# Performance work log

Hardware: AMD Instinct MI355X
Metric: run time of the kernel (lower is better)

## Reference

```python
import jax, jax.numpy as jnp
import numpy as np

H = 1024      # hidden_size
L = 2         # num_layers
V = 32000     # src/tgt vocab
S = 512       # source length
T = 512       # target length
BOS = 0


def _gru_cell(h, x, Wih, Whh, bih, bhh):
    # h,x: [H]; Wih,Whh: [3H,H]; gate order r,z,n (PyTorch convention)
    gi = Wih @ x + bih
    gh = Whh @ h + bhh
    i_r, i_z, i_n = jnp.split(gi, 3)
    h_r, h_z, h_n = jnp.split(gh, 3)
    r = jax.nn.sigmoid(i_r + h_r)
    z = jax.nn.sigmoid(i_z + h_z)
    n = jnp.tanh(i_n + r * h_n)
    return (1.0 - z) * n + z * h


def _run_gru(xs, h0, Wih, Whh, bih, bhh):
    # xs: [T,H] embedded tokens; h0: [L,H]; weights: [L,3H,H]/[L,3H]
    n_layers = Wih.shape[0]

    def step(h, x):
        inp = x
        new_h = []
        for l in range(n_layers):  # small fixed layer loop
            hl = _gru_cell(h[l], inp, Wih[l], Whh[l], bih[l], bhh[l])
            new_h.append(hl)
            inp = hl
        return jnp.stack(new_h), inp  # carry [L,H], emit top-layer hidden

    return jax.lax.scan(step, h0, xs)


def setup_inputs() -> dict:
    key = jax.random.key(0)
    ks = jax.random.split(key, 16)
    sc = 1.0 / np.sqrt(H)

    def gw(k, shape):
        return (jax.random.normal(k, shape, dtype=jnp.float32) * sc)

    return {
        "src_tokens": jax.random.randint(ks[0], (S,), 0, V),
        "tgt_tokens": jax.random.randint(ks[1], (T,), 0, V),
        "src_emb": gw(ks[2], (V, H)),
        "tgt_emb": gw(ks[3], (V, H)),
        "enc_Wih": gw(ks[4], (L, 3 * H, H)),
        "enc_Whh": gw(ks[5], (L, 3 * H, H)),
        "enc_bih": gw(ks[6], (L, 3 * H)),
        "enc_bhh": gw(ks[7], (L, 3 * H)),
        "dec_Wih": gw(ks[8], (L, 3 * H, H)),
        "dec_Whh": gw(ks[9], (L, 3 * H, H)),
        "dec_bih": gw(ks[10], (L, 3 * H)),
        "dec_bhh": gw(ks[11], (L, 3 * H)),
        "out_W": gw(ks[12], (V, H)),
        "out_b": jnp.zeros((V,), dtype=jnp.float32),
    }


def reference(src_tokens, tgt_tokens, src_emb, tgt_emb,
              enc_Wih, enc_Whh, enc_bih, enc_bhh,
              dec_Wih, dec_Whh, dec_bih, dec_bhh,
              out_W, out_b):
    # ---- encoder: embed + L-layer GRU over source ----
    enc_x = src_emb[src_tokens]                       # [S,H]
    h0 = jnp.zeros((enc_Wih.shape[0], src_emb.shape[1]), src_emb.dtype)
    h_enc, _ = _run_gru(enc_x, h0, enc_Wih, enc_Whh, enc_bih, enc_bhh)
    # ---- decoder: teacher-forced inputs [BOS, tgt[:-1]] ----
    dec_in = jnp.concatenate(
        [jnp.array([BOS], dtype=tgt_tokens.dtype), tgt_tokens[:-1]])
    dec_x = tgt_emb[dec_in]                           # [T,H]
    _, dec_top = _run_gru(dec_x, h_enc, dec_Wih, dec_Whh, dec_bih, dec_bhh)
    logits = dec_top @ out_W.T + out_b                # [T,V]
    logp = jax.nn.log_softmax(logits, axis=-1)
    return logp[:, None, None, :]                     # [T,1,1,V] like torch.stack
```

## Files before the change

kernel.cpp:

```cpp
#include <hip/hip_runtime.h>
#include <hip/hip_bf16.h>
#include <math.h>


#define HID 1024
#define NSTEP 512
#define VOCAB 32000
#define SPIN_LIMIT 50000
typedef unsigned long long u64;

__device__ __forceinline__ u64 pack_hv(float v, unsigned tag) {
    return ((u64)tag << 32) | (u64)__float_as_uint(v);
}

__device__ __forceinline__ void poll16(const u64* __restrict__ row, unsigned want,
                                       float* v, int lane) {
    u64 p[16];
    int iter = 0;
    for (;;) {
        bool ok = true;
#pragma unroll
        for (int q = 0; q < 16; ++q) {
            p[q] = __hip_atomic_load((u64*)(row + q * 64 + lane),
                                     __ATOMIC_RELAXED, __HIP_MEMORY_SCOPE_AGENT);
            ok = ok && ((unsigned)(p[q] >> 32) == want);
        }
        if (ok) break;
        if (++iter >= SPIN_LIMIT) {
#pragma unroll
            for (int q = 0; q < 16; ++q) v[q] = __uint_as_float(0x7fc00000u);
            return;
        }
        __builtin_amdgcn_s_sleep(1);
    }
#pragma unroll
    for (int q = 0; q < 16; ++q)
        v[q] = __uint_as_float((unsigned)(p[q] & 0xffffffffu));
}

__global__ __launch_bounds__(256) void gather_embed(
    const int* __restrict__ src_tok, const int* __restrict__ tgt_tok,
    const float* __restrict__ src_emb, const float* __restrict__ tgt_emb,
    float* __restrict__ enc_x, float* __restrict__ dec_x) {
    int b = blockIdx.x, tid = threadIdx.x;
    int tok;
    const float* src;
    float* dst;
    if (b < 512) {
        tok = src_tok[b];
        src = src_emb;
        dst = enc_x + (size_t)b * HID;
    } else {
        int t = b - 512;
        tok = (t == 0) ? 0 : tgt_tok[t - 1];
        src = tgt_emb;
        dst = dec_x + (size_t)t * HID;
    }
    float4 v = *(const float4*)(src + (size_t)tok * HID + tid * 4);
    *(float4*)(dst + tid * 4) = v;
}

__global__ __launch_bounds__(256, 1) void gru_persist(
    const float* __restrict__ enc_x, const float* __restrict__ dec_x,
    const float* __restrict__ eWih, const float* __restrict__ eWhh,
    const float* __restrict__ eBih, const float* __restrict__ eBhh,
    const float* __restrict__ dWih, const float* __restrict__ dWhh,
    const float* __restrict__ dBih, const float* __restrict__ dBhh,
    u64* H0, u64* H1, u64* D0, u64* D1, float* __restrict__ D1f) {
    const int tid = threadIdx.x;
    const int wave = tid >> 6, lane = tid & 63;
    const int role = blockIdx.x >> 7;
    const int wl = blockIdx.x & 127;
    const int j0 = wl * 8;

    __shared__ float dots[48];
    __shared__ float sbias[48];

    float wreg[12][16];
    float hprev = 0.f;

#pragma unroll 1
    for (int phase = 0; phase < 2; ++phase) {
        const bool dec = (phase == 1);
        const float* Wih = (dec ? dWih : eWih) + (size_t)role * 3 * HID * HID;
        const float* Whh = (dec ? dWhh : eWhh) + (size_t)role * 3 * HID * HID;
        const float* bih = (dec ? dBih : eBih) + (size_t)role * 3 * HID;
        const float* bhh = (dec ? dBhh : eBhh) + (size_t)role * 3 * HID;
        u64* hch = dec ? (role ? D1 : D0) : (role ? H1 : H0);
        const unsigned tagOut = dec ? (role ? 4u : 3u) : (role ? 2u : 1u);
        const float* xf = dec ? dec_x : enc_x;
        const u64* xt = dec ? D0 : H0;
        const unsigned tagX = dec ? 3u : 1u;
        const u64* hinit = role ? (H1 + (size_t)(NSTEP - 1) * HID)
                                : (H0 + (size_t)(NSTEP - 1) * HID);
        const unsigned tagInit = role ? 2u : 1u;

        __syncthreads();
#pragma unroll
        for (int r = 0; r < 12; ++r) {
            int R = wave * 12 + r;
            int m = (R < 24) ? R : R - 24;
            const float* base = ((R < 24) ? Wih : Whh) +
                                (size_t)((m >> 3) * HID + j0 + (m & 7)) * HID;
#pragma unroll
            for (int q = 0; q < 16; ++q) wreg[r][q] = base[q * 64 + lane];
        }
        if (tid < 48) {
            int m = (tid < 24) ? tid : tid - 24;
            sbias[tid] = ((tid < 24) ? bih : bhh)[(m >> 3) * HID + j0 + (m & 7)];
        }
        __syncthreads();

#pragma unroll 1
        for (int t = 0; t < NSTEP; ++t) {
            float v[16];
            if (wave < 2) {
                if (role == 0) {
                    const float* xr = xf + (size_t)t * HID;
#pragma unroll
                    for (int q = 0; q < 16; ++q) v[q] = xr[q * 64 + lane];
                } else {
                    poll16(xt + (size_t)t * HID, tagX, v, lane);
                }
            } else {
                if (t > 0) {
                    poll16(hch + (size_t)(t - 1) * HID, tagOut, v, lane);
                } else if (dec) {
                    poll16(hinit, tagInit, v, lane);
                } else {
#pragma unroll
                    for (int q = 0; q < 16; ++q) v[q] = 0.f;
                }
            }

            float part[12];
#pragma unroll
            for (int r = 0; r < 12; ++r) {
                float a = 0.f;
#pragma unroll
                for (int q = 0; q < 16; ++q) a = fmaf(wreg[r][q], v[q], a);
                part[r] = a;
            }
#pragma unroll
            for (int off = 1; off < 64; off <<= 1) {
#pragma unroll
                for (int r = 0; r < 12; ++r) part[r] += __shfl_xor(part[r], off);
            }
            if (lane == 0) {
#pragma unroll
                for (int r = 0; r < 12; ++r) dots[wave * 12 + r] = part[r];
            }
            __syncthreads();

            if (tid < 8) {
                const int jj = tid;
                float ir = dots[jj] + sbias[jj];
                float iz = dots[8 + jj] + sbias[8 + jj];
                float in_ = dots[16 + jj] + sbias[16 + jj];
                float hr = dots[24 + jj] + sbias[24 + jj];
                float hz = dots[32 + jj] + sbias[32 + jj];
                float hn = dots[40 + jj] + sbias[40 + jj];
                float rg = 1.f / (1.f + __expf(-(ir + hr)));
                float zg = 1.f / (1.f + __expf(-(iz + hz)));
                float na = in_ + rg * hn;
                float ng = 2.f / (1.f + __expf(-2.f * na)) - 1.f;
                float hnew = (1.f - zg) * ng + zg * hprev;
                hprev = hnew;
                __hip_atomic_store((u64*)(hch + (size_t)t * HID + j0 + jj),
                                   pack_hv(hnew, tagOut),
                                   __ATOMIC_RELAXED, __HIP_MEMORY_SCOPE_AGENT);
                if (dec && role == 1) D1f[(size_t)t * HID + j0 + jj] = hnew;
            }
            __syncthreads();
        }
    }
}

__global__ __launch_bounds__(256) void gemm_out(
    const float* __restrict__ A, const float* __restrict__ B,
    const float* __restrict__ bias, float* __restrict__ C) {
    const int tid = threadIdx.x;
    const int bi = blockIdx.x;
    const int bv = blockIdx.y;
    const int i0 = bi * 64, v0 = bv * 128;
    __shared__ __align__(16) float As[32 * 68];
    __shared__ __align__(16) float Bs[32 * 132];
    const int tr = tid >> 4, tc = tid & 15;
    float c[4][8] = {};

    for (int kk = 0; kk < HID; kk += 32) {
#pragma unroll
        for (int q = 0; q < 2; q++) {
            int id = tid * 2 + q;
            int r = id >> 3, kq = id & 7;
            float4 a = *(const float4*)&A[(size_t)(i0 + r) * HID + kk + kq * 4];
            As[(kq * 4 + 0) * 68 + r] = a.x;
            As[(kq * 4 + 1) * 68 + r] = a.y;
            As[(kq * 4 + 2) * 68 + r] = a.z;
            As[(kq * 4 + 3) * 68 + r] = a.w;
        }
#pragma unroll
        for (int q = 0; q < 4; q++) {
            int id = tid * 4 + q;
            int vr = id >> 3, kq = id & 7;
            float4 b = *(const float4*)&B[(size_t)(v0 + vr) * HID + kk + kq * 4];
            Bs[(kq * 4 + 0) * 132 + vr] = b.x;
            Bs[(kq * 4 + 1) * 132 + vr] = b.y;
            Bs[(kq * 4 + 2) * 132 + vr] = b.z;
            Bs[(kq * 4 + 3) * 132 + vr] = b.w;
        }
        __syncthreads();
#pragma unroll
        for (int k = 0; k < 32; k++) {
            float4 a4 = *(const float4*)&As[k * 68 + tr * 4];
            float4 b0 = *(const float4*)&Bs[k * 132 + tc * 8];
            float4 b1 = *(const float4*)&Bs[k * 132 + tc * 8 + 4];
            float av[4] = {a4.x, a4.y, a4.z, a4.w};
            float bvv[8] = {b0.x, b0.y, b0.z, b0.w, b1.x, b1.y, b1.z, b1.w};
#pragma unroll
            for (int u = 0; u < 4; u++)
#pragma unroll
                for (int w = 0; w < 8; w++) c[u][w] += av[u] * bvv[w];
        }
        __syncthreads();
    }
    float4 bb0 = *(const float4*)&bias[v0 + tc * 8];
    float4 bb1 = *(const float4*)&bias[v0 + tc * 8 + 4];
#pragma unroll
    for (int u = 0; u < 4; u++) {
        int i = i0 + tr * 4 + u;
        float4 o0 = {c[u][0] + bb0.x, c[u][1] + bb0.y, c[u][2] + bb0.z, c[u][3] + bb0.w};
        float4 o1 = {c[u][4] + bb1.x, c[u][5] + bb1.y, c[u][6] + bb1.z, c[u][7] + bb1.w};
        *(float4*)&C[(size_t)i * VOCAB + v0 + tc * 8] = o0;
        *(float4*)&C[(size_t)i * VOCAB + v0 + tc * 8 + 4] = o1;
    }
}

__global__ __launch_bounds__(256) void log_softmax_inplace(float* __restrict__ C) {
    const int row = blockIdx.x;
    const int tid = threadIdx.x;
    float* p = C + (size_t)row * VOCAB;
    float m = -3.4e38f, s = 0.f;
    for (int idx = tid; idx < VOCAB / 4; idx += 256) {
        float4 x = ((const float4*)p)[idx];
        float xv[4] = {x.x, x.y, x.z, x.w};
#pragma unroll
        for (int u = 0; u < 4; u++) {
            float nm = fmaxf(m, xv[u]);
            s = s * __expf(m - nm) + __expf(xv[u] - nm);
            m = nm;
        }
    }
#pragma unroll
    for (int off = 1; off < 64; off <<= 1) {
        float om = __shfl_xor(m, off);
        float os = __shfl_xor(s, off);
        float nm = fmaxf(m, om);
        s = s * __expf(m - nm) + os * __expf(om - nm);
        m = nm;
    }
    __shared__ float sm[4], ss[4], sL;
    int wv = tid >> 6;
    if ((tid & 63) == 0) { sm[wv] = m; ss[wv] = s; }
    __syncthreads();
    if (tid == 0) {
        float M = sm[0], S = ss[0];
        for (int w = 1; w < 4; w++) {
            float nm = fmaxf(M, sm[w]);
            S = S * __expf(M - nm) + ss[w] * __expf(sm[w] - nm);
            M = nm;
        }
        sL = M + logf(S);
    }
    __syncthreads();
    float L = sL;
    for (int idx = tid; idx < VOCAB / 4; idx += 256) {
        float4 x = ((const float4*)p)[idx];
        x.x -= L; x.y -= L; x.z -= L; x.w -= L;
        ((float4*)p)[idx] = x;
    }
}

extern "C" void kernel_launch(void* const* d_in, const int* in_sizes, int n_in,
                              void* d_out, int out_size, void* d_ws, size_t ws_size,
                              hipStream_t stream) {
    const int* src_tok = (const int*)d_in[0];
    const int* tgt_tok = (const int*)d_in[1];
    const float* src_emb = (const float*)d_in[2];
    const float* tgt_emb = (const float*)d_in[3];
    const float* eWih = (const float*)d_in[4];
    const float* eWhh = (const float*)d_in[5];
    const float* eBih = (const float*)d_in[6];
    const float* eBhh = (const float*)d_in[7];
    const float* dWih = (const float*)d_in[8];
    const float* dWhh = (const float*)d_in[9];
    const float* dBih = (const float*)d_in[10];
    const float* dBhh = (const float*)d_in[11];
    const float* out_W = (const float*)d_in[12];
    const float* out_b = (const float*)d_in[13];
    float* out = (float*)d_out;

    char* ws = (char*)d_ws;
    float* enc_x = (float*)(ws);
    float* dec_x = (float*)(ws + (2ull << 20));
    u64* H0 = (u64*)(ws + (4ull << 20));
    u64* H1 = (u64*)(ws + (8ull << 20));
    u64* D0 = (u64*)(ws + (12ull << 20));
    u64* D1 = (u64*)(ws + (16ull << 20));
    float* D1f = (float*)(ws + (20ull << 20));

    hipMemsetAsync(ws + (4ull << 20), 0, 16ull << 20, stream);

    gather_embed<<<1024, 256, 0, stream>>>(src_tok, tgt_tok, src_emb, tgt_emb, enc_x, dec_x);
    gru_persist<<<256, 256, 0, stream>>>(enc_x, dec_x, eWih, eWhh, eBih, eBhh,
                                         dWih, dWhh, dBih, dBhh, H0, H1, D0, D1, D1f);
    gemm_out<<<dim3(8, 250), 256, 0, stream>>>(D1f, out_W, out_b, out);
    log_softmax_inplace<<<512, 256, 0, stream>>>(out);
}
```

Measured before the change: 3.733 ms.

## Precompute layer-0 input projections with batched GEMM, halve layer-0 recurrent work

Layer 0's input projection Wih·x for every timestep is now computed up front with the existing GEMM kernel for both encoder and decoder. The layer-0 recurrent blocks then load only Whh and do 6 dot rows per wave instead of 12, which shortens the serial critical path. Block-to-role mapping is interleaved across XCDs, and the s_sleep in the poll loop is removed so spinning is tighter. The cost is two extra GEMM launches plus more workspace traffic, and busier polling that adds memory pressure.

```diff
diff --git a/kernel.cpp b/kernel.cpp
--- a/kernel.cpp
+++ b/kernel.cpp
@@ -31,7 +31,6 @@
             for (int q = 0; q < 16; ++q) v[q] = __uint_as_float(0x7fc00000u);
             return;
         }
-        __builtin_amdgcn_s_sleep(1);
     }
 #pragma unroll
     for (int q = 0; q < 16; ++q)
@@ -61,7 +60,7 @@
 }
 
 __global__ __launch_bounds__(256, 1) void gru_persist(
-    const float* __restrict__ enc_x, const float* __restrict__ dec_x,
+    const float* __restrict__ gi_e, const float* __restrict__ gi_d,
     const float* __restrict__ eWih, const float* __restrict__ eWhh,
     const float* __restrict__ eBih, const float* __restrict__ eBhh,
     const float* __restrict__ dWih, const float* __restrict__ dWhh,
@@ -69,8 +68,9 @@
     u64* H0, u64* H1, u64* D0, u64* D1, float* __restrict__ D1f) {
     const int tid = threadIdx.x;
     const int wave = tid >> 6, lane = tid & 63;
-    const int role = blockIdx.x >> 7;
-    const int wl = blockIdx.x & 127;
+    const int xcd = blockIdx.x & 7;
+    const int role = (xcd >= 4) ? 1 : 0;
+    const int wl = (blockIdx.x >> 3) * 4 + (xcd & 3);
     const int j0 = wl * 8;
 
     __shared__ float dots[48];
@@ -88,7 +88,7 @@
         const float* bhh = (dec ? dBhh : eBhh) + (size_t)role * 3 * HID;
         u64* hch = dec ? (role ? D1 : D0) : (role ? H1 : H0);
         const unsigned tagOut = dec ? (role ? 4u : 3u) : (role ? 2u : 1u);
-        const float* xf = dec ? dec_x : enc_x;
+        const float* gi = dec ? gi_d : gi_e;
         const u64* xt = dec ? D0 : H0;
         const unsigned tagX = dec ? 3u : 1u;
         const u64* hinit = role ? (H1 + (size_t)(NSTEP - 1) * HID)
@@ -96,33 +96,44 @@
         const unsigned tagInit = role ? 2u : 1u;
 
         __syncthreads();
-#pragma unroll
-        for (int r = 0; r < 12; ++r) {
-            int R = wave * 12 + r;
-            int m = (R < 24) ? R : R - 24;
-            const float* base = ((R < 24) ? Wih : Whh) +
-                                (size_t)((m >> 3) * HID + j0 + (m & 7)) * HID;
-#pragma unroll
-            for (int q = 0; q < 16; ++q) wreg[r][q] = base[q * 64 + lane];
-        }
-        if (tid < 48) {
-            int m = (tid < 24) ? tid : tid - 24;
-            sbias[tid] = ((tid < 24) ? bih : bhh)[(m >> 3) * HID + j0 + (m & 7)];
+        if (role == 0) {
+#pragma unroll
+            for (int r = 0; r < 6; ++r) {
+                int m = wave * 6 + r;
+                const float* base = Whh + (size_t)((m >> 3) * HID + j0 + (m & 7)) * HID;
+#pragma unroll
+                for (int q = 0; q < 16; ++q) wreg[r][q] = base[q * 64 + lane];
+            }
+            if (tid < 24)
+                sbias[tid] = bhh[(tid >> 3) * HID + j0 + (tid & 7)];
+        } else {
+#pragma unroll
+            for (int r = 0; r < 12; ++r) {
+                int R = wave * 12 + r;
+                int m = (R < 24) ? R : R - 24;
+                const float* base = ((R < 24) ? Wih : Whh) +
+                                    (size_t)((m >> 3) * HID + j0 + (m & 7)) * HID;
+#pragma unroll
+                for (int q = 0; q < 16; ++q) wreg[r][q] = base[q * 64 + lane];
+            }
+            if (tid < 48) {
+                int m = (tid < 24) ? tid : tid - 24;
+                sbias[tid] = ((tid < 24) ? bih : bhh)[(m >> 3) * HID + j0 + (m & 7)];
+            }
         }
         __syncthreads();
 
 #pragma unroll 1
         for (int t = 0; t < NSTEP; ++t) {
-            float v[16];
-            if (wave < 2) {
-                if (role == 0) {
-                    const float* xr = xf + (size_t)t * HID;
-#pragma unroll
-                    for (int q = 0; q < 16; ++q) v[q] = xr[q * 64 + lane];
-                } else {
-                    poll16(xt + (size_t)t * HID, tagX, v, lane);
-                }
-            } else {
+            if (role == 0) {
+                float gir = 0.f, giz = 0.f, gin = 0.f;
+                if (tid < 8) {
+                    const float* gp = gi + (size_t)t * 3 * HID + j0 + tid;
+                    gir = gp[0];
+                    giz = gp[HID];
+                    gin = gp[2 * HID];
+                }
+                float v[16];
                 if (t > 0) {
                     poll16(hch + (size_t)(t - 1) * HID, tagOut, v, lane);
                 } else if (dec) {
@@ -131,54 +142,102 @@
 #pragma unroll
                     for (int q = 0; q < 16; ++q) v[q] = 0.f;
                 }
+                float part[6];
+#pragma unroll
+                for (int r = 0; r < 6; ++r) {
+                    float a = 0.f;
+#pragma unroll
+                    for (int q = 0; q < 16; ++q) a = fmaf(wreg[r][q], v[q], a);
+                    part[r] = a;
+                }
+#pragma unroll
+                for (int off = 1; off < 64; off <<= 1) {
+#pragma unroll
+                    for (int r = 0; r < 6; ++r) part[r] += __shfl_xor(part[r], off);
+                }
+                if (lane == 0) {
+#pragma unroll
+                    for (int r = 0; r < 6; ++r) dots[wave * 6 + r] = part[r];
+                }
+                __syncthreads();
+
+                if (tid < 8) {
+                    const int jj = tid;
+                    float hr = dots[jj] + sbias[jj];
+                    float hz = dots[8 + jj] + sbias[8 + jj];
+                    float hn = dots[16 + jj] + sbias[16 + jj];
+                    float rg = 1.f / (1.f + __expf(-(gir + hr)));
+                    float zg = 1.f / (1.f + __expf(-(giz + hz)));
+                    float na = gin + rg * hn;
+                    float ng = 2.f / (1.f + __expf(-2.f * na)) - 1.f;
+                    float hnew = (1.f - zg) * ng + zg * hprev;
+                    hprev = hnew;
+                    __hip_atomic_store((u64*)(hch + (size_t)t * HID + j0 + jj),
+                                       pack_hv(hnew, tagOut),
+                                       __ATOMIC_RELAXED, __HIP_MEMORY_SCOPE_AGENT);
+                }
+                __syncthreads();
+            } else {
+                float v[16];
+                if (wave < 2) {
+                    poll16(xt + (size_t)t * HID, tagX, v, lane);
+                } else {
+                    if (t > 0) {
+                        poll16(hch + (size_t)(t - 1) * HID, tagOut, v, lane);
+                    } else if (dec) {
+                        poll16(hinit, tagInit, v, lane);
+                    } else {
+#pragma unroll
+                        for (int q = 0; q < 16; ++q) v[q] = 0.f;
+                    }
+                }
+                float part[12];
+#pragma unroll
+                for (int r = 0; r < 12; ++r) {
+                    float a = 0.f;
+#pragma unroll
+                    for (int q = 0; q < 16; ++q) a = fmaf(wreg[r][q], v[q], a);
+                    part[r] = a;
+                }
+#pragma unroll
+                for (int off = 1; off < 64; off <<= 1) {
+#pragma unroll
+                    for (int r = 0; r < 12; ++r) part[r] += __shfl_xor(part[r], off);
+                }
+                if (lane == 0) {
+#pragma unroll
+                    for (int r = 0; r < 12; ++r) dots[wave * 12 + r] = part[r];
+                }
+                __syncthreads();
+
+                if (tid < 8) {
+                    const int jj = tid;
+                    float ir = dots[jj] + sbias[jj];
+                    float iz = dots[8 + jj] + sbias[8 + jj];
+                    float in_ = dots[16 + jj] + sbias[16 + jj];
+                    float hr = dots[24 + jj] + sbias[24 + jj];
+                    float hz = dots[32 + jj] + sbias[32 + jj];
+                    float hn = dots[40 + jj] + sbias[40 + jj];
+                    float rg = 1.f / (1.f + __expf(-(ir + hr)));
+                    float zg = 1.f / (1.f + __expf(-(iz + hz)));
+                    float na = in_ + rg * hn;
+                    float ng = 2.f / (1.f + __expf(-2.f * na)) - 1.f;
+                    float hnew = (1.f - zg) * ng + zg * hprev;
+                    hprev = hnew;
+                    __hip_atomic_store((u64*)(hch + (size_t)t * HID + j0 + jj),
+                                       pack_hv(hnew, tagOut),
+                                       __ATOMIC_RELAXED, __HIP_MEMORY_SCOPE_AGENT);
+                    if (dec) D1f[(size_t)t * HID + j0 + jj] = hnew;
+                }
+                __syncthreads();
             }
-
-            float part[12];
-#pragma unroll
-            for (int r = 0; r < 12; ++r) {
-                float a = 0.f;
-#pragma unroll
-                for (int q = 0; q < 16; ++q) a = fmaf(wreg[r][q], v[q], a);
-                part[r] = a;
-            }
-#pragma unroll
-            for (int off = 1; off < 64; off <<= 1) {
-#pragma unroll
-                for (int r = 0; r < 12; ++r) part[r] += __shfl_xor(part[r], off);
-            }
-            if (lane == 0) {
-#pragma unroll
-                for (int r = 0; r < 12; ++r) dots[wave * 12 + r] = part[r];
-            }
-            __syncthreads();
-
-            if (tid < 8) {
-                const int jj = tid;
-                float ir = dots[jj] + sbias[jj];
-                float iz = dots[8 + jj] + sbias[8 + jj];
-                float in_ = dots[16 + jj] + sbias[16 + jj];
-                float hr = dots[24 + jj] + sbias[24 + jj];
-                float hz = dots[32 + jj] + sbias[32 + jj];
-                float hn = dots[40 + jj] + sbias[40 + jj];
-                float rg = 1.f / (1.f + __expf(-(ir + hr)));
-                float zg = 1.f / (1.f + __expf(-(iz + hz)));
-                float na = in_ + rg * hn;
-                float ng = 2.f / (1.f + __expf(-2.f * na)) - 1.f;
-                float hnew = (1.f - zg) * ng + zg * hprev;
-                hprev = hnew;
-                __hip_atomic_store((u64*)(hch + (size_t)t * HID + j0 + jj),
-                                   pack_hv(hnew, tagOut),
-                                   __ATOMIC_RELAXED, __HIP_MEMORY_SCOPE_AGENT);
-                if (dec && role == 1) D1f[(size_t)t * HID + j0 + jj] = hnew;
-            }
-            __syncthreads();
         }
     }
 }
 
 __global__ __launch_bounds__(256) void gemm_out(
     const float* __restrict__ A, const float* __restrict__ B,
-    const float* __restrict__ bias, float* __restrict__ C) {
+    const float* __restrict__ bias, float* __restrict__ C, int ldc) {
     const int tid = threadIdx.x;
     const int bi = blockIdx.x;
     const int bv = blockIdx.y;
@@ -231,8 +290,8 @@
         int i = i0 + tr * 4 + u;
         float4 o0 = {c[u][0] + bb0.x, c[u][1] + bb0.y, c[u][2] + bb0.z, c[u][3] + bb0.w};
         float4 o1 = {c[u][4] + bb1.x, c[u][5] + bb1.y, c[u][6] + bb1.z, c[u][7] + bb1.w};
-        *(float4*)&C[(size_t)i * VOCAB + v0 + tc * 8] = o0;
-        *(float4*)&C[(size_t)i * VOCAB + v0 + tc * 8 + 4] = o1;
+        *(float4*)&C[(size_t)i * ldc + v0 + tc * 8] = o0;
+        *(float4*)&C[(size_t)i * ldc + v0 + tc * 8 + 4] = o1;
     }
 }
 
@@ -308,12 +367,19 @@
     u64* D0 = (u64*)(ws + (12ull << 20));
     u64* D1 = (u64*)(ws + (16ull << 20));
     float* D1f = (float*)(ws + (20ull << 20));
+    float* gi_e = (float*)(ws + (22ull << 20));
+    float* gi_d = (float*)(ws + (35ull << 20));
 
     hipMemsetAsync(ws + (4ull << 20), 0, 16ull << 20, stream);
 
     gather_embed<<<1024, 256, 0, stream>>>(src_tok, tgt_tok, src_emb, tgt_emb, enc_x, dec_x);
-    gru_persist<<<256, 256, 0, stream>>>(enc_x, dec_x, eWih, eWhh, eBih, eBhh,
+
+    gemm_out<<<dim3(8, 24), 256, 0, stream>>>(enc_x, eWih, eBih, gi_e, 3 * HID);
+    gemm_out<<<dim3(8, 24), 256, 0, stream>>>(dec_x, dWih, dBih, gi_d, 3 * HID);
+
+    gru_persist<<<256, 256, 0, stream>>>(gi_e, gi_d, eWih, eWhh, eBih, eBhh,
                                          dWih, dWhh, dBih, dBhh, H0, H1, D0, D1, D1f);
-    gemm_out<<<dim3(8, 250), 256, 0, stream>>>(D1f, out_W, out_b, out);
+
+    gemm_out<<<dim3(8, 250), 256, 0, stream>>>(D1f, out_W, out_b, out, VOCAB);
     log_softmax_inplace<<<512, 256, 0, stream>>>(out);
 }
```

Measured after the change: 3.960 ms. 1.06x slower.

## Precompute layer-0 input gates, split GRU roles by XCC, pipeline layer-1 input projection

Applied to the files above, without the earlier changes.

Layer-0 input-gate projections for encoder and decoder are hoisted out of the recurrence into batched GEMMs before the persistent kernel. The persistent GRU kernel is restructured so blocks read their XCC id and take roles: layer-0 and layer-1 recurrent cells, plus separate producer blocks that compute layer-1 input projections into a tagged ring buffer. Each cell block now keeps only Whh in registers, stages h through LDS and polls without sleeping, which shortens the per-step critical path. The cost is relying on hardware XCC placement and slot counters to assign roles, with a risk of deadlock or missing roles if the placement differs. The final GEMM reads the tagged D1 buffer directly, so the separate float copy is dropped.

```diff
diff --git a/kernel.cpp b/kernel.cpp
--- a/kernel.cpp
+++ b/kernel.cpp
@@ -6,36 +6,34 @@
 #define HID 1024
 #define NSTEP 512
 #define VOCAB 32000
-#define SPIN_LIMIT 50000
+#define SPIN_LIMIT 20000
 typedef unsigned long long u64;
-
-__device__ __forceinline__ u64 pack_hv(float v, unsigned tag) {
+typedef unsigned int u32;
+
+__device__ __forceinline__ u64 ald(const u64* p) {
+    return __hip_atomic_load(p, __ATOMIC_RELAXED, __HIP_MEMORY_SCOPE_AGENT);
+}
+__device__ __forceinline__ void ast(u64* p, u64 v) {
+    __hip_atomic_store(p, v, __ATOMIC_RELAXED, __HIP_MEMORY_SCOPE_AGENT);
+}
+__device__ __forceinline__ u64 pack_hv(float v, u32 tag) {
     return ((u64)tag << 32) | (u64)__float_as_uint(v);
 }
-
-__device__ __forceinline__ void poll16(const u64* __restrict__ row, unsigned want,
-                                       float* v, int lane) {
-    u64 p[16];
-    int iter = 0;
-    for (;;) {
-        bool ok = true;
-#pragma unroll
-        for (int q = 0; q < 16; ++q) {
-            p[q] = __hip_atomic_load((u64*)(row + q * 64 + lane),
-                                     __ATOMIC_RELAXED, __HIP_MEMORY_SCOPE_AGENT);
-            ok = ok && ((unsigned)(p[q] >> 32) == want);
-        }
-        if (ok) break;
-        if (++iter >= SPIN_LIMIT) {
-#pragma unroll
-            for (int q = 0; q < 16; ++q) v[q] = __uint_as_float(0x7fc00000u);
-            return;
-        }
-        __builtin_amdgcn_s_sleep(1);
-    }
-#pragma unroll
-    for (int q = 0; q < 16; ++q)
-        v[q] = __uint_as_float((unsigned)(p[q] & 0xffffffffu));
+__device__ __forceinline__ float payload(u64 v) {
+    return __uint_as_float((u32)(v & 0xffffffffu));
+}
+__device__ __forceinline__ float sel4(float a, float b, float c, float d, int j) {
+    float ab = (j & 1) ? b : a;
+    float cd = (j & 1) ? d : c;
+    return (j & 2) ? cd : ab;
+}
+__device__ __forceinline__ float sel6(float a, float b, float c, float d, float e,
+                                      float f, int j) {
+    float s01 = (j & 1) ? b : a;
+    float s23 = (j & 1) ? d : c;
+    float s45 = (j & 1) ? f : e;
+    float s03 = (j & 2) ? s23 : s01;
+    return (j & 4) ? s45 : s03;
 }
 
 __global__ __launch_bounds__(256) void gather_embed(
@@ -60,125 +58,226 @@
     *(float4*)(dst + tid * 4) = v;
 }
 
-__global__ __launch_bounds__(256, 1) void gru_persist(
-    const float* __restrict__ enc_x, const float* __restrict__ dec_x,
+__global__ __launch_bounds__(512, 2) void gru_persist(
+    const float* __restrict__ gi_e, const float* __restrict__ gi_d,
     const float* __restrict__ eWih, const float* __restrict__ eWhh,
     const float* __restrict__ eBih, const float* __restrict__ eBhh,
     const float* __restrict__ dWih, const float* __restrict__ dWhh,
     const float* __restrict__ dBih, const float* __restrict__ dBhh,
-    u64* H0, u64* H1, u64* D0, u64* D1, float* __restrict__ D1f) {
+    u64* H0, u64* H1, u64* D0, u64* D1, u64* GIH, u32* cnt) {
     const int tid = threadIdx.x;
     const int wave = tid >> 6, lane = tid & 63;
-    const int role = blockIdx.x >> 7;
-    const int wl = blockIdx.x & 127;
-    const int j0 = wl * 8;
-
-    __shared__ float dots[48];
-    __shared__ float sbias[48];
-
-    float wreg[12][16];
-    float hprev = 0.f;
+
+    __shared__ int s_xcc, s_slot;
+    __shared__ __align__(16) float xbuf[2][HID];
+
+    if (tid == 0) {
+        u32 xcc = (u32)__builtin_amdgcn_s_getreg((31u << 11) | 20u) & 7u;
+        s_xcc = (int)xcc;
+        s_slot = (int)atomicAdd(&cnt[xcc], 1u);
+    }
+    __syncthreads();
+    const int xcc = s_xcc, slot = s_slot;
+
+    int role = -1, rs = 0;
+    if (xcc == 0) {
+        if (slot < 32) { role = 0; rs = slot; }
+        else if (slot < 64) { role = 1; rs = slot - 32; }
+        else if (slot < 128) { role = 2; rs = slot - 64; }
+    } else if (xcc == 1) {
+        if (slot < 32) { role = 1; rs = slot; }
+        else if (slot < 64) { role = 0; rs = slot - 32; }
+        else if (slot < 128) { role = 2; rs = slot - 64; }
+    } else if (xcc == 2) {
+        if (slot < 32) { role = 2; rs = slot; }
+    } else if (xcc == 3) {
+        if (slot < 32) { role = 2; rs = 32 + slot; }
+    }
+    if (role < 0) return;
+
+    if (role < 2) {
+        const int j0 = rs * 32;
+        const int jw = j0 + wave * 4;
+        const int je = jw + (lane & 3);
+        float wreg[12][16];
+        float hprev = 0.f;
 
 #pragma unroll 1
-    for (int phase = 0; phase < 2; ++phase) {
-        const bool dec = (phase == 1);
-        const float* Wih = (dec ? dWih : eWih) + (size_t)role * 3 * HID * HID;
-        const float* Whh = (dec ? dWhh : eWhh) + (size_t)role * 3 * HID * HID;
-        const float* bih = (dec ? dBih : eBih) + (size_t)role * 3 * HID;
-        const float* bhh = (dec ? dBhh : eBhh) + (size_t)role * 3 * HID;
-        u64* hch = dec ? (role ? D1 : D0) : (role ? H1 : H0);
-        const unsigned tagOut = dec ? (role ? 4u : 3u) : (role ? 2u : 1u);
-        const float* xf = dec ? dec_x : enc_x;
-        const u64* xt = dec ? D0 : H0;
-        const unsigned tagX = dec ? 3u : 1u;
-        const u64* hinit = role ? (H1 + (size_t)(NSTEP - 1) * HID)
-                                : (H0 + (size_t)(NSTEP - 1) * HID);
-        const unsigned tagInit = role ? 2u : 1u;
-
-        __syncthreads();
-#pragma unroll
-        for (int r = 0; r < 12; ++r) {
-            int R = wave * 12 + r;
-            int m = (R < 24) ? R : R - 24;
-            const float* base = ((R < 24) ? Wih : Whh) +
-                                (size_t)((m >> 3) * HID + j0 + (m & 7)) * HID;
-#pragma unroll
-            for (int q = 0; q < 16; ++q) wreg[r][q] = base[q * 64 + lane];
-        }
-        if (tid < 48) {
-            int m = (tid < 24) ? tid : tid - 24;
-            sbias[tid] = ((tid < 24) ? bih : bhh)[(m >> 3) * HID + j0 + (m & 7)];
-        }
-        __syncthreads();
+        for (int p = 0; p < 2; ++p) {
+            const float* Whh = (p ? dWhh : eWhh) + (size_t)role * 3 * HID * HID;
+            const float* bhh = (p ? dBhh : eBhh) + (size_t)role * 3 * HID;
+            u64* hch = p ? (role ? D1 : D0) : (role ? H1 : H0);
+            const u32 tagOut = p ? (role ? 4u : 3u) : (role ? 2u : 1u);
+            u64* prevch = role ? H1 : H0;
+            const u32 tagPrev = role ? 2u : 1u;
+            const float* gilin = p ? gi_d : gi_e;
+
+#pragma unroll
+            for (int g = 0; g < 3; ++g)
+#pragma unroll
+                for (int jj = 0; jj < 4; ++jj) {
+                    const float* base = Whh + (size_t)(g * HID + jw + jj) * HID;
+#pragma unroll
+                    for (int q = 0; q < 16; ++q)
+                        wreg[g * 4 + jj][q] = base[q * 64 + lane];
+                }
+            float bR = 0.f, bZ = 0.f, bN = 0.f;
+            if (lane < 4) {
+                bR = bhh[je];
+                bZ = bhh[HID + je];
+                bN = bhh[2 * HID + je];
+            }
 
 #pragma unroll 1
-        for (int t = 0; t < NSTEP; ++t) {
-            float v[16];
-            if (wave < 2) {
-                if (role == 0) {
-                    const float* xr = xf + (size_t)t * HID;
-#pragma unroll
-                    for (int q = 0; q < 16; ++q) v[q] = xr[q * 64 + lane];
-                } else {
-                    poll16(xt + (size_t)t * HID, tagX, v, lane);
-                }
-            } else {
-                if (t > 0) {
-                    poll16(hch + (size_t)(t - 1) * HID, tagOut, v, lane);
-                } else if (dec) {
-                    poll16(hinit, tagInit, v, lane);
-                } else {
-#pragma unroll
-                    for (int q = 0; q < 16; ++q) v[q] = 0.f;
+            for (int t = 0; t < NSTEP; ++t) {
+                float* xb = xbuf[t & 1];
+                float g0 = 0.f, g1 = 0.f, g2 = 0.f;
+                u64 q0 = 0, q1 = 0, q2 = 0;
+                const u32 wantGI = 0x50000000u | ((u32)p << 24) | (u32)t;
+                const u64* gp = GIH + (size_t)(t & 255) * 3 * HID + je;
+                if (lane < 4) {
+                    if (role == 0) {
+                        const float* gl = gilin + (size_t)t * 3 * HID + je;
+                        g0 = gl[0]; g1 = gl[HID]; g2 = gl[2 * HID];
+                    } else {
+                        q0 = ald(gp); q1 = ald(gp + HID); q2 = ald(gp + 2 * HID);
+                    }
+                }
+                {
+                    const int qa = 2 * wave, qb = qa + 1;
+                    if (t == 0 && p == 0) {
+                        xb[qa * 64 + lane] = 0.f;
+                        xb[qb * 64 + lane] = 0.f;
+                    } else {
+                        const u64* src = (t > 0) ? (hch + (size_t)(t - 1) * HID)
+                                                 : (prevch + (size_t)(NSTEP - 1) * HID);
+                        const u32 want = (t > 0) ? tagOut : tagPrev;
+                        const u64* pa = src + qa * 64 + lane;
+                        const u64* pb = src + qb * 64 + lane;
+                        u64 va, vb;
+                        int it = 0;
+                        for (;;) {
+                            va = ald(pa);
+                            vb = ald(pb);
+                            if ((u32)(va >> 32) == want && (u32)(vb >> 32) == want) break;
+                            if (++it >= SPIN_LIMIT) { va = vb = 0x7fc00000u; break; }
+                        }
+                        xb[qa * 64 + lane] = payload(va);
+                        xb[qb * 64 + lane] = payload(vb);
+                    }
+                }
+                __syncthreads();
+
+                float part[12] = {0.f, 0.f, 0.f, 0.f, 0.f, 0.f,
+                                  0.f, 0.f, 0.f, 0.f, 0.f, 0.f};
+#pragma unroll
+                for (int q = 0; q < 16; ++q) {
+                    float vq = xb[q * 64 + lane];
+#pragma unroll
+                    for (int rr = 0; rr < 12; ++rr)
+                        part[rr] = fmaf(wreg[rr][q], vq, part[rr]);
+                }
+#pragma unroll
+                for (int off = 1; off < 64; off <<= 1)
+#pragma unroll
+                    for (int rr = 0; rr < 12; ++rr)
+                        part[rr] += __shfl_xor(part[rr], off);
+
+                if (lane < 4) {
+                    const int jj = lane;
+                    float hr = sel4(part[0], part[1], part[2], part[3], jj) + bR;
+                    float hz = sel4(part[4], part[5], part[6], part[7], jj) + bZ;
+                    float hn = sel4(part[8], part[9], part[10], part[11], jj) + bN;
+                    float gir, giz, gin;
+                    if (role == 0) {
+                        gir = g0; giz = g1; gin = g2;
+                    } else {
+                        int it = 0;
+                        while ((u32)(q0 >> 32) != wantGI || (u32)(q1 >> 32) != wantGI ||
+                               (u32)(q2 >> 32) != wantGI) {
+                            if (++it >= SPIN_LIMIT) { q0 = q1 = q2 = 0x7fc00000u; break; }
+                            q0 = ald(gp); q1 = ald(gp + HID); q2 = ald(gp + 2 * HID);
+                        }
+                        gir = payload(q0); giz = payload(q1); gin = payload(q2);
+                    }
+                    float rg = 1.f / (1.f + __expf(-(gir + hr)));
+                    float zg = 1.f / (1.f + __expf(-(giz + hz)));
+                    float na = gin + rg * hn;
+                    float ng = 2.f / (1.f + __expf(-2.f * na)) - 1.f;
+                    float hnew = (1.f - zg) * ng + zg * hprev;
+                    hprev = hnew;
+                    ast(hch + (size_t)t * HID + je, pack_hv(hnew, tagOut));
                 }
             }
-
-            float part[12];
-#pragma unroll
-            for (int r = 0; r < 12; ++r) {
-                float a = 0.f;
-#pragma unroll
-                for (int q = 0; q < 16; ++q) a = fmaf(wreg[r][q], v[q], a);
-                part[r] = a;
+        }
+    } else {
+        const int mb = rs * 48;
+        float wreg[6][16];
+#pragma unroll 1
+        for (int p = 0; p < 2; ++p) {
+            const float* Wih1 = (p ? dWih : eWih) + (size_t)3 * HID * HID;
+            const float* bih1 = (p ? dBih : eBih) + 3 * HID;
+            const u64* srcc = p ? D0 : H0;
+            const u32 wantH = p ? 3u : 1u;
+#pragma unroll
+            for (int rr = 0; rr < 6; ++rr) {
+                int m = mb + wave * 6 + rr;
+                const float* base = Wih1 + (size_t)m * HID;
+#pragma unroll
+                for (int q = 0; q < 16; ++q) wreg[rr][q] = base[q * 64 + lane];
             }
-#pragma unroll
-            for (int off = 1; off < 64; off <<= 1) {
-#pragma unroll
-                for (int r = 0; r < 12; ++r) part[r] += __shfl_xor(part[r], off);
+            float bi = 0.f;
+            if (lane < 6) bi = bih1[mb + wave * 6 + lane];
+
+#pragma unroll 1
+            for (int t = 0; t < NSTEP; ++t) {
+                float* xb = xbuf[t & 1];
+                const int qa = 2 * wave, qb = qa + 1;
+                const u64* pa = srcc + (size_t)t * HID + qa * 64 + lane;
+                const u64* pb = srcc + (size_t)t * HID + qb * 64 + lane;
+                u64 va, vb;
+                int it = 0;
+                for (;;) {
+                    va = ald(pa);
+                    vb = ald(pb);
+                    if ((u32)(va >> 32) == wantH && (u32)(vb >> 32) == wantH) break;
+                    if (++it >= SPIN_LIMIT) { va = vb = 0x7fc00000u; break; }
+                    __builtin_amdgcn_s_sleep(8);
+                }
+                xb[qa * 64 + lane] = payload(va);
+                xb[qb * 64 + lane] = payload(vb);
+                __syncthreads();
+
+                float part[6] = {0.f, 0.f, 0.f, 0.f, 0.f, 0.f};
+#pragma unroll
+                for (int q = 0; q < 16; ++q) {
+                    float vq = xb[q * 64 + lane];
+#pragma unroll
+                    for (int rr = 0; rr < 6; ++rr)
+                        part[rr] = fmaf(wreg[rr][q], vq, part[rr]);
+                }
+#pragma unroll
+                for (int off = 1; off < 64; off <<= 1)
+#pragma unroll
+                    for (int rr = 0; rr < 6; ++rr)
+                        part[rr] += __shfl_xor(part[rr], off);
+
+                if (lane < 6) {
+                    int m = mb + wave * 6 + lane;
+                    float val = sel6(part[0], part[1], part[2], part[3], part[4],
+                                     part[5], lane) + bi;
+                    ast(GIH + (size_t)(t & 255) * 3 * HID + m,
+                        pack_hv(val, 0x50000000u | ((u32)p << 24) | (u32)t));
+                }
             }
-            if (lane == 0) {
-#pragma unroll
-                for (int r = 0; r < 12; ++r) dots[wave * 12 + r] = part[r];
-            }
-            __syncthreads();
-
-            if (tid < 8) {
-                const int jj = tid;
-                float ir = dots[jj] + sbias[jj];
-                float iz = dots[8 + jj] + sbias[8 + jj];
-                float in_ = dots[16 + jj] + sbias[16 + jj];
-                float hr = dots[24 + jj] + sbias[24 + jj];
-                float hz = dots[32 + jj] + sbias[32 + jj];
-                float hn = dots[40 + jj] + sbias[40 + jj];
-                float rg = 1.f / (1.f + __expf(-(ir + hr)));
-                float zg = 1.f / (1.f + __expf(-(iz + hz)));
-                float na = in_ + rg * hn;
-                float ng = 2.f / (1.f + __expf(-2.f * na)) - 1.f;
-                float hnew = (1.f - zg) * ng + zg * hprev;
-                hprev = hnew;
-                __hip_atomic_store((u64*)(hch + (size_t)t * HID + j0 + jj),
-                                   pack_hv(hnew, tagOut),
-                                   __ATOMIC_RELAXED, __HIP_MEMORY_SCOPE_AGENT);
-                if (dec && role == 1) D1f[(size_t)t * HID + j0 + jj] = hnew;
-            }
-            __syncthreads();
-        }
-    }
-}
-
-__global__ __launch_bounds__(256) void gemm_out(
-    const float* __restrict__ A, const float* __restrict__ B,
-    const float* __restrict__ bias, float* __restrict__ C) {
+        }
+    }
+}
+
+template <int ATAG>
+__global__ __launch_bounds__(256) void gemm_k(
+    const void* __restrict__ Ap, const float* __restrict__ B,
+    const float* __restrict__ bias, float* __restrict__ C, int ldc) {
     const int tid = threadIdx.x;
     const int bi = blockIdx.x;
     const int bv = blockIdx.y;
@@ -193,7 +292,15 @@
         for (int q = 0; q < 2; q++) {
             int id = tid * 2 + q;
             int r = id >> 3, kq = id & 7;
-            float4 a = *(const float4*)&A[(size_t)(i0 + r) * HID + kk + kq * 4];
+            float4 a;
+            if constexpr (ATAG) {
+                const u64* Au = (const u64*)Ap + (size_t)(i0 + r) * HID + kk + kq * 4;
+                a = make_float4(payload(Au[0]), payload(Au[1]), payload(Au[2]),
+                                payload(Au[3]));
+            } else {
+                a = *(const float4*)((const float*)Ap + (size_t)(i0 + r) * HID + kk +
+                                     kq * 4);
+            }
             As[(kq * 4 + 0) * 68 + r] = a.x;
             As[(kq * 4 + 1) * 68 + r] = a.y;
             As[(kq * 4 + 2) * 68 + r] = a.z;
@@ -231,8 +338,8 @@
         int i = i0 + tr * 4 + u;
         float4 o0 = {c[u][0] + bb0.x, c[u][1] + bb0.y, c[u][2] + bb0.z, c[u][3] + bb0.w};
         float4 o1 = {c[u][4] + bb1.x, c[u][5] + bb1.y, c[u][6] + bb1.z, c[u][7] + bb1.w};
-        *(float4*)&C[(size_t)i * VOCAB + v0 + tc * 8] = o0;
-        *(float4*)&C[(size_t)i * VOCAB + v0 + tc * 8 + 4] = o1;
+        *(float4*)&C[(size_t)i * ldc + v0 + tc * 8] = o0;
+        *(float4*)&C[(size_t)i * ldc + v0 + tc * 8 + 4] = o1;
     }
 }
 
@@ -307,13 +414,22 @@
     u64* H1 = (u64*)(ws + (8ull << 20));
     u64* D0 = (u64*)(ws + (12ull << 20));
     u64* D1 = (u64*)(ws + (16ull << 20));
-    float* D1f = (float*)(ws + (20ull << 20));
-
-    hipMemsetAsync(ws + (4ull << 20), 0, 16ull << 20, stream);
-
-    gather_embed<<<1024, 256, 0, stream>>>(src_tok, tgt_tok, src_emb, tgt_emb, enc_x, dec_x);
-    gru_persist<<<256, 256, 0, stream>>>(enc_x, dec_x, eWih, eWhh, eBih, eBhh,
-                                         dWih, dWhh, dBih, dBhh, H0, H1, D0, D1, D1f);
-    gemm_out<<<dim3(8, 250), 256, 0, stream>>>(D1f, out_W, out_b, out);
+    u64* GIH = (u64*)(ws + (20ull << 20));
+    u32* cnt = (u32*)(ws + (26ull << 20));
+    float* gi_e = (float*)(ws + (27ull << 20));
+    float* gi_d = (float*)(ws + (33ull << 20));
+
+    hipMemsetAsync(ws + (4ull << 20), 0, 23ull << 20, stream);
+
+    gather_embed<<<1024, 256, 0, stream>>>(src_tok, tgt_tok, src_emb, tgt_emb,
+                                           enc_x, dec_x);
+    gemm_k<0><<<dim3(8, 24), 256, 0, stream>>>(enc_x, eWih, eBih, gi_e, 3 * HID);
+    gemm_k<0><<<dim3(8, 24), 256, 0, stream>>>(dec_x, dWih, dBih, gi_d, 3 * HID);
+
+    gru_persist<<<256, 512, 0, stream>>>(gi_e, gi_d, eWih, eWhh, eBih, eBhh,
+                                         dWih, dWhh, dBih, dBhh, H0, H1, D0, D1,
+                                         GIH, cnt);
+
+    gemm_k<1><<<dim3(8, 250), 256, 0, stream>>>(D1, out_W, out_b, out, VOCAB);
     log_softmax_inplace<<<512, 256, 0, stream>>>(out);
 }
```

Result: slower. 4.852 ms (+30.0%).

## Give each wave whole hidden units to remove block barriers in GRU step

Applied to the files above, without the earlier changes.

Restructures the persistent GRU so each wave owns two hidden units and computes all six gate dot products for them. Each wave reduces with shuffles and applies the gate math itself, so the shared-memory staging and both per-step __syncthreads are gone. The recurrent h dot is issued first, before the x poll, and the s_sleep in the poll loop is removed for tighter spinning. In exchange every wave now polls all 1024 h values and x values each step, which raises global/L2 polling traffic, and the busy spin may add memory contention.

```diff
diff --git a/kernel.cpp b/kernel.cpp
--- a/kernel.cpp
+++ b/kernel.cpp
@@ -8,12 +8,22 @@
 #define VOCAB 32000
 #define SPIN_LIMIT 50000
 typedef unsigned long long u64;
-
-__device__ __forceinline__ u64 pack_hv(float v, unsigned tag) {
+typedef unsigned int u32;
+
+__device__ __forceinline__ u64 ald(const u64* p) {
+    return __hip_atomic_load(p, __ATOMIC_RELAXED, __HIP_MEMORY_SCOPE_AGENT);
+}
+__device__ __forceinline__ void ast(u64* p, u64 v) {
+    __hip_atomic_store(p, v, __ATOMIC_RELAXED, __HIP_MEMORY_SCOPE_AGENT);
+}
+__device__ __forceinline__ u64 pack_hv(float v, u32 tag) {
     return ((u64)tag << 32) | (u64)__float_as_uint(v);
 }
-
-__device__ __forceinline__ void poll16(const u64* __restrict__ row, unsigned want,
+__device__ __forceinline__ float payload(u64 v) {
+    return __uint_as_float((u32)(v & 0xffffffffu));
+}
+
+__device__ __forceinline__ void poll16(const u64* __restrict__ row, u32 want,
                                        float* v, int lane) {
     u64 p[16];
     int iter = 0;
@@ -21,9 +31,8 @@
         bool ok = true;
 #pragma unroll
         for (int q = 0; q < 16; ++q) {
-            p[q] = __hip_atomic_load((u64*)(row + q * 64 + lane),
-                                     __ATOMIC_RELAXED, __HIP_MEMORY_SCOPE_AGENT);
-            ok = ok && ((unsigned)(p[q] >> 32) == want);
+            p[q] = ald(row + q * 64 + lane);
+            ok = ok && ((u32)(p[q] >> 32) == want);
         }
         if (ok) break;
         if (++iter >= SPIN_LIMIT) {
@@ -31,11 +40,9 @@
             for (int q = 0; q < 16; ++q) v[q] = __uint_as_float(0x7fc00000u);
             return;
         }
-        __builtin_amdgcn_s_sleep(1);
-    }
-#pragma unroll
-    for (int q = 0; q < 16; ++q)
-        v[q] = __uint_as_float((unsigned)(p[q] & 0xffffffffu));
+    }
+#pragma unroll
+    for (int q = 0; q < 16; ++q) v[q] = payload(p[q]);
 }
 
 __global__ __launch_bounds__(256) void gather_embed(
@@ -70,115 +77,115 @@
     const int tid = threadIdx.x;
     const int wave = tid >> 6, lane = tid & 63;
     const int role = blockIdx.x >> 7;
-    const int wl = blockIdx.x & 127;
-    const int j0 = wl * 8;
-
-    __shared__ float dots[48];
-    __shared__ float sbias[48];
+    const int jw = (blockIdx.x & 127) * 8 + wave * 2;
+    const int jsel = jw + (lane & 1);
 
     float wreg[12][16];
     float hprev = 0.f;
 
 #pragma unroll 1
-    for (int phase = 0; phase < 2; ++phase) {
-        const bool dec = (phase == 1);
-        const float* Wih = (dec ? dWih : eWih) + (size_t)role * 3 * HID * HID;
-        const float* Whh = (dec ? dWhh : eWhh) + (size_t)role * 3 * HID * HID;
-        const float* bih = (dec ? dBih : eBih) + (size_t)role * 3 * HID;
-        const float* bhh = (dec ? dBhh : eBhh) + (size_t)role * 3 * HID;
-        u64* hch = dec ? (role ? D1 : D0) : (role ? H1 : H0);
-        const unsigned tagOut = dec ? (role ? 4u : 3u) : (role ? 2u : 1u);
-        const float* xf = dec ? dec_x : enc_x;
-        const u64* xt = dec ? D0 : H0;
-        const unsigned tagX = dec ? 3u : 1u;
-        const u64* hinit = role ? (H1 + (size_t)(NSTEP - 1) * HID)
-                                : (H0 + (size_t)(NSTEP - 1) * HID);
-        const unsigned tagInit = role ? 2u : 1u;
-
-        __syncthreads();
-#pragma unroll
-        for (int r = 0; r < 12; ++r) {
-            int R = wave * 12 + r;
-            int m = (R < 24) ? R : R - 24;
-            const float* base = ((R < 24) ? Wih : Whh) +
-                                (size_t)((m >> 3) * HID + j0 + (m & 7)) * HID;
-#pragma unroll
-            for (int q = 0; q < 16; ++q) wreg[r][q] = base[q * 64 + lane];
-        }
-        if (tid < 48) {
-            int m = (tid < 24) ? tid : tid - 24;
-            sbias[tid] = ((tid < 24) ? bih : bhh)[(m >> 3) * HID + j0 + (m & 7)];
-        }
-        __syncthreads();
+    for (int p = 0; p < 2; ++p) {
+        const float* Wih = (p ? dWih : eWih) + (size_t)role * 3 * HID * HID;
+        const float* Whh = (p ? dWhh : eWhh) + (size_t)role * 3 * HID * HID;
+        const float* bih = (p ? dBih : eBih) + (size_t)role * 3 * HID;
+        const float* bhh = (p ? dBhh : eBhh) + (size_t)role * 3 * HID;
+        u64* hch = p ? (role ? D1 : D0) : (role ? H1 : H0);
+        const u32 tagOut = p ? (role ? 4u : 3u) : (role ? 2u : 1u);
+        u64* prevch = role ? H1 : H0;
+        const u32 tagPrev = role ? 2u : 1u;
+        const float* xf = p ? dec_x : enc_x;
+        const u64* xt = p ? D0 : H0;
+        const u32 tagX = p ? 3u : 1u;
+
+#pragma unroll
+        for (int e = 0; e < 2; ++e)
+#pragma unroll
+            for (int m = 0; m < 6; ++m) {
+                int g = (m < 3) ? m : m - 3;
+                const float* base = ((m < 3) ? Wih : Whh) +
+                                    (size_t)(g * HID + jw + e) * HID;
+#pragma unroll
+                for (int q = 0; q < 16; ++q)
+                    wreg[e * 6 + m][q] = base[q * 64 + lane];
+            }
+        const float bIR = bih[jsel], bIZ = bih[HID + jsel], bIN = bih[2 * HID + jsel];
+        const float bHR = bhh[jsel], bHZ = bhh[HID + jsel], bHN = bhh[2 * HID + jsel];
 
 #pragma unroll 1
         for (int t = 0; t < NSTEP; ++t) {
-            float v[16];
-            if (wave < 2) {
+            float part[12] = {0.f, 0.f, 0.f, 0.f, 0.f, 0.f,
+                              0.f, 0.f, 0.f, 0.f, 0.f, 0.f};
+            {
+                float h[16];
+                if (t == 0 && p == 0) {
+#pragma unroll
+                    for (int q = 0; q < 16; ++q) h[q] = 0.f;
+                } else {
+                    const u64* src = (t > 0) ? (hch + (size_t)(t - 1) * HID)
+                                             : (prevch + (size_t)(NSTEP - 1) * HID);
+                    poll16(src, (t > 0) ? tagOut : tagPrev, h, lane);
+                }
+#pragma unroll
+                for (int q = 0; q < 16; ++q) {
+                    float hq = h[q];
+#pragma unroll
+                    for (int e = 0; e < 2; ++e)
+#pragma unroll
+                        for (int m = 3; m < 6; ++m)
+                            part[e * 6 + m] = fmaf(wreg[e * 6 + m][q], hq,
+                                                   part[e * 6 + m]);
+                }
+            }
+            {
+                float x[16];
                 if (role == 0) {
                     const float* xr = xf + (size_t)t * HID;
 #pragma unroll
-                    for (int q = 0; q < 16; ++q) v[q] = xr[q * 64 + lane];
+                    for (int q = 0; q < 16; ++q) x[q] = xr[q * 64 + lane];
                 } else {
-                    poll16(xt + (size_t)t * HID, tagX, v, lane);
+                    poll16(xt + (size_t)t * HID, tagX, x, lane);
                 }
-            } else {
-                if (t > 0) {
-                    poll16(hch + (size_t)(t - 1) * HID, tagOut, v, lane);
-                } else if (dec) {
-                    poll16(hinit, tagInit, v, lane);
-                } else {
-#pragma unroll
-                    for (int q = 0; q < 16; ++q) v[q] = 0.f;
+#pragma unroll
+                for (int q = 0; q < 16; ++q) {
+                    float xq = x[q];
+#pragma unroll
+                    for (int e = 0; e < 2; ++e)
+#pragma unroll
+                        for (int m = 0; m < 3; ++m)
+                            part[e * 6 + m] = fmaf(wreg[e * 6 + m][q], xq,
+                                                   part[e * 6 + m]);
                 }
             }
-
-            float part[12];
-#pragma unroll
-            for (int r = 0; r < 12; ++r) {
-                float a = 0.f;
-#pragma unroll
-                for (int q = 0; q < 16; ++q) a = fmaf(wreg[r][q], v[q], a);
-                part[r] = a;
+#pragma unroll
+            for (int off = 1; off < 64; off <<= 1)
+#pragma unroll
+                for (int rr = 0; rr < 12; ++rr)
+                    part[rr] += __shfl_xor(part[rr], off);
+
+            const bool e1 = (lane & 1) != 0;
+            float ir = (e1 ? part[6] : part[0]) + bIR;
+            float iz = (e1 ? part[7] : part[1]) + bIZ;
+            float in_ = (e1 ? part[8] : part[2]) + bIN;
+            float hr = (e1 ? part[9] : part[3]) + bHR;
+            float hz = (e1 ? part[10] : part[4]) + bHZ;
+            float hn = (e1 ? part[11] : part[5]) + bHN;
+            float rg = 1.f / (1.f + __expf(-(ir + hr)));
+            float zg = 1.f / (1.f + __expf(-(iz + hz)));
+            float na = in_ + rg * hn;
+            float ng = 2.f / (1.f + __expf(-2.f * na)) - 1.f;
+            float hnew = (1.f - zg) * ng + zg * hprev;
+            hprev = hnew;
+            if (lane < 2) {
+                ast(hch + (size_t)t * HID + jsel, pack_hv(hnew, tagOut));
+                if (p && role) D1f[(size_t)t * HID + jsel] = hnew;
             }
-#pragma unroll
-            for (int off = 1; off < 64; off <<= 1) {
-#pragma unroll
-                for (int r = 0; r < 12; ++r) part[r] += __shfl_xor(part[r], off);
-            }
-            if (lane == 0) {
-#pragma unroll
-                for (int r = 0; r < 12; ++r) dots[wave * 12 + r] = part[r];
-            }
-            __syncthreads();
-
-            if (tid < 8) {
-                const int jj = tid;
-                float ir = dots[jj] + sbias[jj];
-                float iz = dots[8 + jj] + sbias[8 + jj];
-                float in_ = dots[16 + jj] + sbias[16 + jj];
-                float hr = dots[24 + jj] + sbias[24 + jj];
-                float hz = dots[32 + jj] + sbias[32 + jj];
-                float hn = dots[40 + jj] + sbias[40 + jj];
-                float rg = 1.f / (1.f + __expf(-(ir + hr)));
-                float zg = 1.f / (1.f + __expf(-(iz + hz)));
-                float na = in_ + rg * hn;
-                float ng = 2.f / (1.f + __expf(-2.f * na)) - 1.f;
-                float hnew = (1.f - zg) * ng + zg * hprev;
-                hprev = hnew;
-                __hip_atomic_store((u64*)(hch + (size_t)t * HID + j0 + jj),
-                                   pack_hv(hnew, tagOut),
-                                   __ATOMIC_RELAXED, __HIP_MEMORY_SCOPE_AGENT);
-                if (dec && role == 1) D1f[(size_t)t * HID + j0 + jj] = hnew;
-            }
-            __syncthreads();
         }
     }
 }
 
 __global__ __launch_bounds__(256) void gemm_out(
     const float* __restrict__ A, const float* __restrict__ B,
-    const float* __restrict__ bias, float* __restrict__ C) {
+    const float* __restrict__ bias, float* __restrict__ C, int ldc) {
     const int tid = threadIdx.x;
     const int bi = blockIdx.x;
     const int bv = blockIdx.y;
@@ -231,8 +238,8 @@
         int i = i0 + tr * 4 + u;
         float4 o0 = {c[u][0] + bb0.x, c[u][1] + bb0.y, c[u][2] + bb0.z, c[u][3] + bb0.w};
         float4 o1 = {c[u][4] + bb1.x, c[u][5] + bb1.y, c[u][6] + bb1.z, c[u][7] + bb1.w};
-        *(float4*)&C[(size_t)i * VOCAB + v0 + tc * 8] = o0;
-        *(float4*)&C[(size_t)i * VOCAB + v0 + tc * 8 + 4] = o1;
+        *(float4*)&C[(size_t)i * ldc + v0 + tc * 8] = o0;
+        *(float4*)&C[(size_t)i * ldc + v0 + tc * 8 + 4] = o1;
     }
 }
 
@@ -311,9 +318,10 @@
 
     hipMemsetAsync(ws + (4ull << 20), 0, 16ull << 20, stream);
 
-    gather_embed<<<1024, 256, 0, stream>>>(src_tok, tgt_tok, src_emb, tgt_emb, enc_x, dec_x);
+    gather_embed<<<1024, 256, 0, stream>>>(src_tok, tgt_tok, src_emb, tgt_emb,
+                                           enc_x, dec_x);
     gru_persist<<<256, 256, 0, stream>>>(enc_x, dec_x, eWih, eWhh, eBih, eBhh,
                                          dWih, dWhh, dBih, dBhh, H0, H1, D0, D1, D1f);
-    gemm_out<<<dim3(8, 250), 256, 0, stream>>>(D1f, out_W, out_b, out);
+    gemm_out<<<dim3(8, 250), 256, 0, stream>>>(D1f, out_W, out_b, out, VOCAB);
     log_softmax_inplace<<<512, 256, 0, stream>>>(out);
 }
```

Result: slower. 7.122 ms (+90.8%).
